# Optimization experiments

Measured on AMD Instinct MI355X. Metric: run time of the kernel, lower is better.

## Reference

```python
import jax, jax.numpy as jnp
import numpy as np

EPS = 1e-6
NUM_HEADS = 16


def setup_inputs() -> dict:
    key = jax.random.key(0)
    ks = jax.random.split(key, 11)
    B, S, E = 2, 2048, 1024
    sc = 1.0 / np.sqrt(E)
    return {
        "x": jax.random.normal(ks[0], (B, S, E), dtype=jnp.float32),
        "Wq": jax.random.normal(ks[1], (E, E), dtype=jnp.float32) * sc,
        "bq": jax.random.normal(ks[2], (E,), dtype=jnp.float32) * 0.01,
        "Wk": jax.random.normal(ks[3], (E, E), dtype=jnp.float32) * sc,
        "bk": jax.random.normal(ks[4], (E,), dtype=jnp.float32) * 0.01,
        "Wv": jax.random.normal(ks[5], (E, E), dtype=jnp.float32) * sc,
        "bv": jax.random.normal(ks[6], (E,), dtype=jnp.float32) * 0.01,
        "Wp": jax.random.normal(ks[7], (E, E), dtype=jnp.float32) * sc,
        "bp": jax.random.normal(ks[8], (E,), dtype=jnp.float32) * 0.01,
        "gain": jax.random.uniform(ks[9], (E,), dtype=jnp.float32),
        "beta": jax.random.normal(ks[10], (E,), dtype=jnp.float32),
    }


def _layer_norm(x, gain, beta):
    # torch: (x - mean) / (std + eps) * gain + bias, std with Bessel correction
    mean = jnp.mean(x, axis=-1, keepdims=True)
    std = jnp.std(x, axis=-1, keepdims=True, ddof=1)
    return (x - mean) / (std + EPS) * gain + beta


def reference(x, Wq, bq, Wk, bk, Wv, bv, Wp, bp, gain, beta):
    B, S, E = x.shape
    H = NUM_HEADS
    D = E // H
    # QKV projections, split heads: [B,S,E] -> [B,H,S,D]
    def heads(y):
        return y.reshape(B, S, H, D).transpose(0, 2, 1, 3)
    q = heads(x @ Wq + bq)
    k = heads(x @ Wk + bk)
    v = heads(x @ Wv + bv)
    # scores [B,H,S,S], mask=None path (no causal mask applied in forward)
    scores = jnp.einsum("bhid,bhjd->bhij", q, k) / jnp.sqrt(jnp.float32(D))
    attn = jax.nn.softmax(scores, axis=-1)  # dropout is identity at eval
    y = jnp.einsum("bhij,bhjd->bhid", attn, v)
    y = y.transpose(0, 2, 1, 3).reshape(B, S, E)
    return _layer_norm(y @ Wp + bp, gain, beta)
```

## Files before the change

### kernel.cpp

```cpp
#include <hip/hip_runtime.h>
#include <hip/hip_bf16.h>
#include <math.h>

constexpr int Bc = 2;
constexpr int Sc = 2048;
constexpr int Ec = 1024;
constexpr int Hc = 16;
constexpr int Dc = 64;

typedef __attribute__((ext_vector_type(8))) short short8;
typedef __attribute__((ext_vector_type(4))) short short4v;
typedef __attribute__((ext_vector_type(2))) int int2v;
typedef __attribute__((ext_vector_type(4))) float f32x4;

__device__ inline unsigned short f2bf(float x) {
    __hip_bfloat16 h = __float2bfloat16(x);
    return *reinterpret_cast<unsigned short*>(&h);
}

__device__ inline float bf2f(unsigned short u) {
    unsigned int v = (unsigned int)u << 16;
    return __builtin_bit_cast(float, v);
}

__device__ inline f32x4 mfma16(short8 a, short8 b, f32x4 c) {
    return __builtin_amdgcn_mfma_f32_16x16x32_bf16(a, b, c, 0, 0, 0);
}

__device__ inline f32x4 mfma16k16(short4v a, short4v b, f32x4 c) {
#if __has_builtin(__builtin_amdgcn_mfma_f32_16x16x16bf16_1k)
    return __builtin_amdgcn_mfma_f32_16x16x16bf16_1k(a, b, c, 0, 0, 0);
#else
    f32x4 d;
    asm("v_mfma_f32_16x16x16_bf16 %0, %1, %2, %3"
        : "=v"(d) : "v"(a), "v"(b), "v"(c));
    return d;
#endif
}

__device__ inline float exp2_fast(float x) {
    float r;
    asm("v_exp_f32 %0, %1" : "=v"(r) : "v"(x));
    return r;
}

__device__ inline int cvt_pk_bf16(float lo, float hi) {
    int r;
    asm("v_cvt_pk_bf16_f32 %0, %1, %2" : "=v"(r) : "v"(lo), "v"(hi));
    return r;
}

__device__ inline void gload_lds16(const unsigned short* gsrc, unsigned short* ldst) {
    __builtin_amdgcn_global_load_lds(
        (const __attribute__((address_space(1))) unsigned int*)(const void*)gsrc,
        (__attribute__((address_space(3))) unsigned int*)(void*)ldst,
        16, 0, 0);
}

__global__ __launch_bounds__(256) void convert_x_kernel(
    const float* __restrict__ X, unsigned short* __restrict__ Xb, int total8)
{
    int i = blockIdx.x * 256 + threadIdx.x;
    if (i >= total8) return;
    const float4* src = (const float4*)(X + (size_t)i * 8);
    float4 a = src[0], b = src[1];
    short8 o;
    o[0] = f2bf(a.x); o[1] = f2bf(a.y); o[2] = f2bf(a.z); o[3] = f2bf(a.w);
    o[4] = f2bf(b.x); o[5] = f2bf(b.y); o[6] = f2bf(b.z); o[7] = f2bf(b.w);
    *(short8*)(Xb + (size_t)i * 8) = o;
}

__global__ __launch_bounds__(256) void transpose_w_kernel(
    const float* __restrict__ W0, const float* __restrict__ W1,
    const float* __restrict__ W2, const float* __restrict__ W3,
    unsigned short* __restrict__ T0, unsigned short* __restrict__ T1,
    unsigned short* __restrict__ T2, unsigned short* __restrict__ T3)
{
    __shared__ unsigned short Ls[64][72];
    const float* W; unsigned short* T;
    switch (blockIdx.z) {
        case 0: W = W0; T = T0; break;
        case 1: W = W1; T = T1; break;
        case 2: W = W2; T = T2; break;
        default: W = W3; T = T3; break;
    }
    const int n0 = blockIdx.x * 64, k0 = blockIdx.y * 64;
    const int t = threadIdx.x;
    {
        int k = t >> 2, nb = (t & 3) * 16;
        const float* src = W + (size_t)(k0 + k) * Ec + n0 + nb;
#pragma unroll
        for (int j = 0; j < 16; ++j) Ls[k][nb + j] = f2bf(src[j]);
    }
    __syncthreads();
    {
        int n = t >> 2, kb = (t & 3) * 16;
        short8 o0, o1;
#pragma unroll
        for (int j = 0; j < 8; ++j) { o0[j] = Ls[kb + j][n]; o1[j] = Ls[kb + 8 + j][n]; }
        unsigned short* dst = T + (size_t)(n0 + n) * Ec + k0 + kb;
        *(short8*)dst = o0;
        *(short8*)(dst + 8) = o1;
    }
}

constexpr int BM = 128, BK = 64;

template<int BNt>
__device__ __forceinline__ void gemm_core_t(
    const unsigned short* __restrict__ A, const unsigned short* __restrict__ Bt,
    const float* __restrict__ bias, float* __restrict__ Cf,
    unsigned short* __restrict__ Cb, int M, int N, int K, int mode, float oscale)
{
    constexpr int NW = BNt / 32;
    constexpr int WN = BNt / 2;
    constexpr int CH = (BM + BNt) / 8;
    constexpr int PW = CH / 4;
    __shared__ unsigned short lds[2][(BM + BNt) * BK];
    const int tid = threadIdx.x, lane = tid & 63, wid = tid >> 6;
    const int c16 = lane & 15, g = lane >> 4;
    const int wr = wid >> 1, wc = wid & 1;
    const int row0 = blockIdx.y * BM, col0 = blockIdx.x * BNt;

    const int rsub = lane >> 3;
    const int colE = ((lane & 7) ^ rsub) * 8;

    f32x4 acc[4][NW] = {};

    auto stage = [&](int buf, int k0) {
        unsigned short* Ab = &lds[buf][0];
        unsigned short* Bb = &lds[buf][BM * BK];
#pragma unroll
        for (int i = 0; i < PW; ++i) {
            int c = wid * PW + i;
            if (c < 16) {
                const unsigned short* src = A + (size_t)(row0 + c * 8 + rsub) * K + k0 + colE;
                gload_lds16(src, Ab + c * 512);
            } else {
                int c2 = c - 16;
                const unsigned short* src = Bt + (size_t)(col0 + c2 * 8 + rsub) * K + k0 + colE;
                gload_lds16(src, Bb + c2 * 512);
            }
        }
    };

    stage(0, 0);
    __syncthreads();
    int cur = 0;
    const int NT = K / BK;
    for (int t = 0; t < NT; ++t) {
        if (t + 1 < NT) stage(cur ^ 1, (t + 1) * BK);
        const unsigned short* Ab = &lds[cur][0];
        const unsigned short* Bb = &lds[cur][BM * BK];
#pragma unroll
        for (int kk = 0; kk < 2; ++kk) {
            const int cb = ((kk * 64 + g * 16) ^ ((c16 & 7) << 4)) >> 1;
            short8 af[4], bfr[NW];
#pragma unroll
            for (int m = 0; m < 4; ++m) {
                int row = wr * 64 + m * 16 + c16;
                af[m] = *(const short8*)(Ab + row * BK + cb);
            }
#pragma unroll
            for (int n = 0; n < NW; ++n) {
                int row = wc * WN + n * 16 + c16;
                bfr[n] = *(const short8*)(Bb + row * BK + cb);
            }
#pragma unroll
            for (int m = 0; m < 4; ++m)
#pragma unroll
                for (int n = 0; n < NW; ++n)
                    acc[m][n] = mfma16(af[m], bfr[n], acc[m][n]);
        }
        __syncthreads();
        cur ^= 1;
    }

#pragma unroll
    for (int m = 0; m < 4; ++m) {
#pragma unroll
        for (int n = 0; n < NW; ++n) {
            int gc = col0 + wc * WN + n * 16 + c16;
            float bi = bias[gc];
            if (mode == 2) {
                int h = gc >> 6, d = gc & (Dc - 1);
                int s0 = row0 + wr * 64 + m * 16 + g * 4;
                int b = s0 >> 11, s = s0 & (Sc - 1);
                short4v pk;
#pragma unroll
                for (int r = 0; r < 4; ++r)
                    pk[r] = (short)f2bf((acc[m][n][r] + bi) * oscale);
                *(short4v*)&Cb[(((size_t)b * Hc + h) * Dc + d) * Sc + s] = pk;
            } else {
#pragma unroll
                for (int r = 0; r < 4; ++r) {
                    int gr = row0 + wr * 64 + m * 16 + g * 4 + r;
                    float v = (acc[m][n][r] + bi) * oscale;
                    if (mode == 0) {
                        Cf[(size_t)gr * N + gc] = v;
                    } else {
                        int b = gr >> 11, s = gr & (Sc - 1);
                        int h = gc >> 6, d = gc & (Dc - 1);
                        Cb[(((size_t)b * Hc + h) * Sc + s) * Dc + d] = f2bf(v);
                    }
                }
            }
        }
    }
}

__global__ __launch_bounds__(256) void gemm_mfma_kernel(
    const unsigned short* __restrict__ A, const unsigned short* __restrict__ Bt,
    const float* __restrict__ bias, float* __restrict__ Cf, int M, int N, int K)
{
    gemm_core_t<64>(A, Bt, bias, Cf, nullptr, M, N, K, 0, 1.0f);
}

__global__ __launch_bounds__(256) void qkv_gemm_kernel(
    const unsigned short* __restrict__ A,
    const unsigned short* __restrict__ WqT, const unsigned short* __restrict__ WkT,
    const unsigned short* __restrict__ WvT,
    const float* __restrict__ bq, const float* __restrict__ bk,
    const float* __restrict__ bv,
    unsigned short* __restrict__ Qb, unsigned short* __restrict__ Kb,
    unsigned short* __restrict__ Vt, int M, int N, int K, float sl2e)
{
    if (blockIdx.z == 0)      gemm_core_t<128>(A, WqT, bq, nullptr, Qb, M, N, K, 1, sl2e);
    else if (blockIdx.z == 1) gemm_core_t<128>(A, WkT, bk, nullptr, Kb, M, N, K, 1, 1.0f);
    else                      gemm_core_t<128>(A, WvT, bv, nullptr, Vt, M, N, K, 2, 1.0f);
}

__global__ __launch_bounds__(256) void attn_mfma_kernel(
    const unsigned short* __restrict__ Q, const unsigned short* __restrict__ K,
    const unsigned short* __restrict__ Vt,
    unsigned short* __restrict__ Op0, unsigned short* __restrict__ Op1,
    float* __restrict__ ls)
{
    __shared__ __align__(16) unsigned short lds[2][2][64 * 64];

    const int tid  = threadIdx.x;
    const int lane = tid & 63, wid = tid >> 6;
    const int g = lane >> 4, c16 = lane & 15;
    const int bh = blockIdx.x;
    const int qw = blockIdx.y * 128 + wid * 32;
    const int ks = blockIdx.z;
    const int kbase = ks * (Sc / 2);
    const size_t base = (size_t)bh * Sc * Dc;

    short8 bq[2][2];
#pragma unroll
    for (int u = 0; u < 2; ++u) {
        const unsigned short* Qp = Q + base + (size_t)(qw + u * 16 + c16) * Dc;
        bq[u][0] = *(const short8*)(Qp + g * 8);
        bq[u][1] = *(const short8*)(Qp + 32 + g * 8);
    }

    const int rsub = lane >> 3;
    const int srcoffE = 8 * ((lane & 7) ^ rsub);
    const int row0g = (wid * 2 + 0) * 8 + rsub;
    const int row1g = (wid * 2 + 1) * 8 + rsub;

    const unsigned short* kg0 = K  + base + (size_t)(kbase + row0g) * Dc + srcoffE;
    const unsigned short* kg1 = K  + base + (size_t)(kbase + row1g) * Dc + srcoffE;
    const unsigned short* vg0 = Vt + base + (size_t)row0g * Sc + kbase + srcoffE;
    const unsigned short* vg1 = Vt + base + (size_t)row1g * Sc + kbase + srcoffE;

    f32x4 o[2][4] = {};
    float psacc[2] = {0.f, 0.f};

    auto stage = [&](unsigned short* kbuf, unsigned short* vbuf) {
        gload_lds16(kg0, kbuf + (wid * 2 + 0) * 512);
        gload_lds16(kg1, kbuf + (wid * 2 + 1) * 512);
        gload_lds16(vg0, vbuf + (wid * 2 + 0) * 512);
        gload_lds16(vg1, vbuf + (wid * 2 + 1) * 512);
        kg0 += 64 * Dc; kg1 += 64 * Dc;
        vg0 += 64;      vg1 += 64;
    };

    const int sw = (c16 & 7) << 4;

    auto compute = [&](const unsigned short* kbuf, const unsigned short* vbuf) {
        const char* kbc = (const char*)kbuf;
        const char* vbc = (const char*)vbuf;

        f32x4 c[2][4];
        __builtin_amdgcn_s_setprio(1);
#pragma unroll
        for (int ct = 0; ct < 4; ++ct) {
            const int kr = ct * 16 + c16;
            short8 alo = *(const short8*)(kbc + kr * 128 + ((16 * g) ^ sw));
            short8 ahi = *(const short8*)(kbc + kr * 128 + ((64 + 16 * g) ^ sw));
            f32x4 z0 = {}, z1 = {};
            z0 = mfma16(alo, bq[0][0], z0);
            c[0][ct] = mfma16(ahi, bq[0][1], z0);
            z1 = mfma16(alo, bq[1][0], z1);
            c[1][ct] = mfma16(ahi, bq[1][1], z1);
        }
        __builtin_amdgcn_s_setprio(0);

        short4v pbv[2][4];
#pragma unroll
        for (int u = 0; u < 2; ++u) {
            float ps = 0.f;
#pragma unroll
            for (int ct = 0; ct < 4; ++ct) {
                float p0 = exp2_fast(c[u][ct][0]);
                float p1 = exp2_fast(c[u][ct][1]);
                float p2 = exp2_fast(c[u][ct][2]);
                float p3 = exp2_fast(c[u][ct][3]);
                ps += (p0 + p1) + (p2 + p3);
                int2v w;
                w[0] = cvt_pk_bf16(p0, p1);
                w[1] = cvt_pk_bf16(p2, p3);
                pbv[u][ct] = __builtin_bit_cast(short4v, w);
            }
            psacc[u] += ps;
        }

        __builtin_amdgcn_s_setprio(1);
#pragma unroll
        for (int dt = 0; dt < 4; ++dt) {
            const int drow = dt * 16 + c16;
#pragma unroll
            for (int ct = 0; ct < 4; ++ct) {
                short4v va = *(const short4v*)(vbc + drow * 128 + ((ct * 32 + 8 * g) ^ sw));
                o[0][dt] = mfma16k16(va, pbv[0][ct], o[0][dt]);
                o[1][dt] = mfma16k16(va, pbv[1][ct], o[1][dt]);
            }
        }
        __builtin_amdgcn_s_setprio(0);
    };

    unsigned short* k0b = &lds[0][0][0]; unsigned short* v0b = &lds[0][1][0];
    unsigned short* k1b = &lds[1][0][0]; unsigned short* v1b = &lds[1][1][0];

    constexpr int NT = (Sc / 2) / 64;
    stage(k0b, v0b);
    for (int kt = 0; kt < NT; kt += 2) {
        asm volatile("s_waitcnt vmcnt(0)" ::: "memory");
        __builtin_amdgcn_s_barrier();
        __builtin_amdgcn_sched_barrier(0);
        if (kt + 1 < NT) stage(k1b, v1b);
        compute(k0b, v0b);
        asm volatile("s_waitcnt vmcnt(0)" ::: "memory");
        __builtin_amdgcn_s_barrier();
        __builtin_amdgcn_sched_barrier(0);
        if (kt + 2 < NT) stage(k0b, v0b);
        compute(k1b, v1b);
    }

    const int b = bh >> 4, h = bh & (Hc - 1);
    unsigned short* Op = ks ? Op1 : Op0;
#pragma unroll
    for (int u = 0; u < 2; ++u) {
        float ps = psacc[u];
        ps += __shfl_xor(ps, 16);
        ps += __shfl_xor(ps, 32);
        const int qg = qw + u * 16 + c16;
        unsigned short* yrow = Op + ((size_t)b * Sc + qg) * Ec + h * Dc;
#pragma unroll
        for (int dt = 0; dt < 4; ++dt)
#pragma unroll
            for (int r = 0; r < 4; ++r)
                yrow[dt * 16 + g * 4 + r] = f2bf(o[u][dt][r]);
        if (g == 0)
            ls[((size_t)ks * (Bc * Hc) + bh) * Sc + qg] = ps;
    }
}

__global__ __launch_bounds__(256) void combine_kernel(
    const unsigned short* __restrict__ Op0, unsigned short* __restrict__ Op1,
    const float* __restrict__ ls)
{
    const int i = blockIdx.x * 256 + threadIdx.x;
    const int e4 = i * 4;
    const int bq = e4 >> 10;
    const int e  = e4 & 1023;
    const int h  = e >> 6;
    const int b  = bq >> 11, q = bq & (Sc - 1);
    const int bh = b * Hc + h;

    float l0 = ls[(size_t)bh * Sc + q];
    float l1 = ls[((size_t)(Bc * Hc) + bh) * Sc + q];
    float inv = 1.0f / (l0 + l1);

    short4v a = *(const short4v*)(Op0 + e4);
    short4v c = *(const short4v*)(Op1 + e4);
    short4v o;
#pragma unroll
    for (int j = 0; j < 4; ++j)
        o[j] = (short)f2bf((bf2f((unsigned short)a[j]) +
                            bf2f((unsigned short)c[j])) * inv);
    *(short4v*)(Op1 + e4) = o;
}

__global__ __launch_bounds__(256) void ln_kernel(
    const float* __restrict__ Z, const float* __restrict__ gain,
    const float* __restrict__ beta, float* __restrict__ out)
{
    __shared__ float red0[4];
    __shared__ float red1[4];
    const int row = blockIdx.x;
    const int t = threadIdx.x;
    const float4* z4 = (const float4*)(Z + (size_t)row * Ec);
    float4 v = z4[t];

    float s = v.x + v.y + v.z + v.w;
#pragma unroll
    for (int off = 32; off > 0; off >>= 1) s += __shfl_down(s, off);
    if ((t & 63) == 0) red0[t >> 6] = s;
    __syncthreads();
    float mean = (red0[0] + red0[1] + red0[2] + red0[3]) * (1.0f / Ec);

    float dx = v.x - mean; float vs = dx * dx;
    dx = v.y - mean; vs += dx * dx;
    dx = v.z - mean; vs += dx * dx;
    dx = v.w - mean; vs += dx * dx;
#pragma unroll
    for (int off = 32; off > 0; off >>= 1) vs += __shfl_down(vs, off);
    if ((t & 63) == 0) red1[t >> 6] = vs;
    __syncthreads();
    float var = (red1[0] + red1[1] + red1[2] + red1[3]) * (1.0f / (Ec - 1));
    float inv = 1.0f / (sqrtf(var) + 1e-6f);

    float4 g = ((const float4*)gain)[t];
    float4 bb = ((const float4*)beta)[t];
    float4 o;
    o.x = (v.x - mean) * inv * g.x + bb.x;
    o.y = (v.y - mean) * inv * g.y + bb.y;
    o.z = (v.z - mean) * inv * g.z + bb.z;
    o.w = (v.w - mean) * inv * g.w + bb.w;
    ((float4*)(out + (size_t)row * Ec))[t] = o;
}

extern "C" void kernel_launch(void* const* d_in, const int* in_sizes, int n_in,
                              void* d_out, int out_size, void* d_ws, size_t ws_size,
                              hipStream_t stream)
{
    const float* x    = (const float*)d_in[0];
    const float* Wq   = (const float*)d_in[1];
    const float* bq   = (const float*)d_in[2];
    const float* Wk   = (const float*)d_in[3];
    const float* bk   = (const float*)d_in[4];
    const float* Wv   = (const float*)d_in[5];
    const float* bv   = (const float*)d_in[6];
    const float* Wp   = (const float*)d_in[7];
    const float* bp   = (const float*)d_in[8];
    const float* gain = (const float*)d_in[9];
    const float* beta = (const float*)d_in[10];

    const int M = Bc * Sc;
    const size_t MK  = (size_t)M * Ec;
    const size_t EE  = (size_t)Ec * Ec;

    unsigned short* xb  = (unsigned short*)d_ws;
    unsigned short* wqt = xb + MK;
    unsigned short* wkt = wqt + EE;
    unsigned short* wvt = wkt + EE;
    unsigned short* wpt = wvt + EE;
    unsigned short* qb  = wpt + EE;
    unsigned short* kb  = qb + MK;
    unsigned short* vt  = kb + MK;
    unsigned short* yb  = vt + MK;
    float* ls = (float*)(yb + MK);

    float* z = (float*)qb;

    const float sl2e = 0.125f * 1.44269504f;

    convert_x_kernel<<<(int)(MK / 8 / 256), 256, 0, stream>>>(x, xb, (int)(MK / 8));
    transpose_w_kernel<<<dim3(Ec / 64, Ec / 64, 4), 256, 0, stream>>>(
        Wq, Wk, Wv, Wp, wqt, wkt, wvt, wpt);

    dim3 qkv_grid(Ec / 128, M / BM, 3);
    qkv_gemm_kernel<<<qkv_grid, 256, 0, stream>>>(
        xb, wqt, wkt, wvt, bq, bk, bv, qb, kb, vt, M, Ec, Ec, sl2e);

    dim3 attn_grid(Bc * Hc, Sc / 128, 2);
    attn_mfma_kernel<<<attn_grid, 256, 0, stream>>>(qb, kb, vt, xb, yb, ls);

    combine_kernel<<<(int)(MK / 4 / 256), 256, 0, stream>>>(xb, yb, ls);

    dim3 proj_grid(Ec / 64, M / BM);
    gemm_mfma_kernel<<<proj_grid, 256, 0, stream>>>(yb, wpt, bp, z, M, Ec, Ec);

    ln_kernel<<<M, 256, 0, stream>>>(z, gain, beta, (float*)d_out);
}
```

Before: 137.1 us.

## Double query rows per attention wave and interleave QK/exp per key tile

Each wave now handles 64 query rows instead of 32, halving the attention grid in the query dimension so every staged K/V tile in LDS is reused across twice as many queries. The QK^T MFMAs and the exp2/bf16 packing are now interleaved per key column tile rather than computed in two separate phases. This cuts K/V global and LDS traffic per query but doubles the accumulator and Q register footprint, which may lower occupancy. The grid shrinks to 512 blocks, which could leave compute units underused.

```diff
diff --git a/kernel.cpp b/kernel.cpp
--- a/kernel.cpp
+++ b/kernel.cpp
@@ -242,14 +242,14 @@
     const int lane = tid & 63, wid = tid >> 6;
     const int g = lane >> 4, c16 = lane & 15;
     const int bh = blockIdx.x;
-    const int qw = blockIdx.y * 128 + wid * 32;
+    const int qw = blockIdx.y * 256 + wid * 64;
     const int ks = blockIdx.z;
     const int kbase = ks * (Sc / 2);
     const size_t base = (size_t)bh * Sc * Dc;
 
-    short8 bq[2][2];
-#pragma unroll
-    for (int u = 0; u < 2; ++u) {
+    short8 bq[4][2];
+#pragma unroll
+    for (int u = 0; u < 4; ++u) {
         const unsigned short* Qp = Q + base + (size_t)(qw + u * 16 + c16) * Dc;
         bq[u][0] = *(const short8*)(Qp + g * 8);
         bq[u][1] = *(const short8*)(Qp + 32 + g * 8);
@@ -265,8 +265,8 @@
     const unsigned short* vg0 = Vt + base + (size_t)row0g * Sc + kbase + srcoffE;
     const unsigned short* vg1 = Vt + base + (size_t)row1g * Sc + kbase + srcoffE;
 
-    f32x4 o[2][4] = {};
-    float psacc[2] = {0.f, 0.f};
+    f32x4 o[4][4] = {};
+    float psacc[4] = {0.f, 0.f, 0.f, 0.f};
 
     auto stage = [&](unsigned short* kbuf, unsigned short* vbuf) {
         gload_lds16(kg0, kbuf + (wid * 2 + 0) * 512);
@@ -283,38 +283,33 @@
         const char* kbc = (const char*)kbuf;
         const char* vbc = (const char*)vbuf;
 
-        f32x4 c[2][4];
-        __builtin_amdgcn_s_setprio(1);
+        short4v pbv[4][4];
 #pragma unroll
         for (int ct = 0; ct < 4; ++ct) {
             const int kr = ct * 16 + c16;
             short8 alo = *(const short8*)(kbc + kr * 128 + ((16 * g) ^ sw));
             short8 ahi = *(const short8*)(kbc + kr * 128 + ((64 + 16 * g) ^ sw));
-            f32x4 z0 = {}, z1 = {};
-            z0 = mfma16(alo, bq[0][0], z0);
-            c[0][ct] = mfma16(ahi, bq[0][1], z0);
-            z1 = mfma16(alo, bq[1][0], z1);
-            c[1][ct] = mfma16(ahi, bq[1][1], z1);
-        }
-        __builtin_amdgcn_s_setprio(0);
-
-        short4v pbv[2][4];
-#pragma unroll
-        for (int u = 0; u < 2; ++u) {
-            float ps = 0.f;
-#pragma unroll
-            for (int ct = 0; ct < 4; ++ct) {
-                float p0 = exp2_fast(c[u][ct][0]);
-                float p1 = exp2_fast(c[u][ct][1]);
-                float p2 = exp2_fast(c[u][ct][2]);
-                float p3 = exp2_fast(c[u][ct][3]);
-                ps += (p0 + p1) + (p2 + p3);
+            f32x4 c4[4];
+            __builtin_amdgcn_s_setprio(1);
+#pragma unroll
+            for (int u = 0; u < 4; ++u) {
+                f32x4 z = {};
+                z = mfma16(alo, bq[u][0], z);
+                c4[u] = mfma16(ahi, bq[u][1], z);
+            }
+            __builtin_amdgcn_s_setprio(0);
+#pragma unroll
+            for (int u = 0; u < 4; ++u) {
+                float p0 = exp2_fast(c4[u][0]);
+                float p1 = exp2_fast(c4[u][1]);
+                float p2 = exp2_fast(c4[u][2]);
+                float p3 = exp2_fast(c4[u][3]);
+                psacc[u] += (p0 + p1) + (p2 + p3);
                 int2v w;
                 w[0] = cvt_pk_bf16(p0, p1);
                 w[1] = cvt_pk_bf16(p2, p3);
                 pbv[u][ct] = __builtin_bit_cast(short4v, w);
             }
-            psacc[u] += ps;
         }
 
         __builtin_amdgcn_s_setprio(1);
@@ -324,8 +319,9 @@
 #pragma unroll
             for (int ct = 0; ct < 4; ++ct) {
                 short4v va = *(const short4v*)(vbc + drow * 128 + ((ct * 32 + 8 * g) ^ sw));
-                o[0][dt] = mfma16k16(va, pbv[0][ct], o[0][dt]);
-                o[1][dt] = mfma16k16(va, pbv[1][ct], o[1][dt]);
+#pragma unroll
+                for (int u = 0; u < 4; ++u)
+                    o[u][dt] = mfma16k16(va, pbv[u][ct], o[u][dt]);
             }
         }
         __builtin_amdgcn_s_setprio(0);
@@ -352,7 +348,7 @@
     const int b = bh >> 4, h = bh & (Hc - 1);
     unsigned short* Op = ks ? Op1 : Op0;
 #pragma unroll
-    for (int u = 0; u < 2; ++u) {
+    for (int u = 0; u < 4; ++u) {
         float ps = psacc[u];
         ps += __shfl_xor(ps, 16);
         ps += __shfl_xor(ps, 32);
@@ -476,7 +472,7 @@
     qkv_gemm_kernel<<<qkv_grid, 256, 0, stream>>>(
         xb, wqt, wkt, wvt, bq, bk, bv, qb, kb, vt, M, Ec, Ec, sl2e);
 
-    dim3 attn_grid(Bc * Hc, Sc / 128, 2);
+    dim3 attn_grid(Bc * Hc, Sc / 256, 2);
     attn_mfma_kernel<<<attn_grid, 256, 0, stream>>>(qb, kb, vt, xb, yb, ls);
 
     combine_kernel<<<(int)(MK / 4 / 256), 256, 0, stream>>>(xb, yb, ls);
```

Result: slower. 141.8 us (+3.4%).

## Drop split-K attention and combine pass; merge prep kernels into one launch

Applied to the files above, without the earlier changes.

The attention kernel no longer splits the key dimension across two blocks. Each block now walks all 2048 keys and normalizes its output by the row sum before writing, so the partial-output buffers and the separate combine kernel go away. The x conversion and weight transposes are also fused into a single prep launch. This cuts a kernel launch plus the extra global traffic for partial outputs and sums, but the attention grid shrinks from 1024 to 512 blocks, which lowers parallelism on a large-CU GPU.

```diff
diff --git a/kernel.cpp b/kernel.cpp
--- a/kernel.cpp
+++ b/kernel.cpp
@@ -16,11 +16,6 @@
 __device__ inline unsigned short f2bf(float x) {
     __hip_bfloat16 h = __float2bfloat16(x);
     return *reinterpret_cast<unsigned short*>(&h);
-}
-
-__device__ inline float bf2f(unsigned short u) {
-    unsigned int v = (unsigned int)u << 16;
-    return __builtin_bit_cast(float, v);
 }
 
 __device__ inline f32x4 mfma16(short8 a, short8 b, f32x4 c) {
@@ -57,35 +52,35 @@
         16, 0, 0);
 }
 
-__global__ __launch_bounds__(256) void convert_x_kernel(
-    const float* __restrict__ X, unsigned short* __restrict__ Xb, int total8)
-{
-    int i = blockIdx.x * 256 + threadIdx.x;
-    if (i >= total8) return;
-    const float4* src = (const float4*)(X + (size_t)i * 8);
-    float4 a = src[0], b = src[1];
-    short8 o;
-    o[0] = f2bf(a.x); o[1] = f2bf(a.y); o[2] = f2bf(a.z); o[3] = f2bf(a.w);
-    o[4] = f2bf(b.x); o[5] = f2bf(b.y); o[6] = f2bf(b.z); o[7] = f2bf(b.w);
-    *(short8*)(Xb + (size_t)i * 8) = o;
-}
-
-__global__ __launch_bounds__(256) void transpose_w_kernel(
+__global__ __launch_bounds__(256) void prep_kernel(
+    const float* __restrict__ X, unsigned short* __restrict__ Xb,
     const float* __restrict__ W0, const float* __restrict__ W1,
     const float* __restrict__ W2, const float* __restrict__ W3,
     unsigned short* __restrict__ T0, unsigned short* __restrict__ T1,
     unsigned short* __restrict__ T2, unsigned short* __restrict__ T3)
 {
     __shared__ unsigned short Ls[64][72];
+    const int bid = blockIdx.x, t = threadIdx.x;
+    if (bid < 2048) {
+        int i = bid * 256 + t;
+        const float4* src = (const float4*)(X + (size_t)i * 8);
+        float4 a = src[0], b = src[1];
+        short8 o;
+        o[0] = f2bf(a.x); o[1] = f2bf(a.y); o[2] = f2bf(a.z); o[3] = f2bf(a.w);
+        o[4] = f2bf(b.x); o[5] = f2bf(b.y); o[6] = f2bf(b.z); o[7] = f2bf(b.w);
+        *(short8*)(Xb + (size_t)i * 8) = o;
+        return;
+    }
+    const int tt = bid - 2048;
     const float* W; unsigned short* T;
-    switch (blockIdx.z) {
+    switch (tt >> 8) {
         case 0: W = W0; T = T0; break;
         case 1: W = W1; T = T1; break;
         case 2: W = W2; T = T2; break;
         default: W = W3; T = T3; break;
     }
-    const int n0 = blockIdx.x * 64, k0 = blockIdx.y * 64;
-    const int t = threadIdx.x;
+    const int rem = tt & 255;
+    const int n0 = (rem & 15) * 64, k0 = (rem >> 4) * 64;
     {
         int k = t >> 2, nb = (t & 3) * 16;
         const float* src = W + (size_t)(k0 + k) * Ec + n0 + nb;
@@ -232,9 +227,7 @@
 
 __global__ __launch_bounds__(256) void attn_mfma_kernel(
     const unsigned short* __restrict__ Q, const unsigned short* __restrict__ K,
-    const unsigned short* __restrict__ Vt,
-    unsigned short* __restrict__ Op0, unsigned short* __restrict__ Op1,
-    float* __restrict__ ls)
+    const unsigned short* __restrict__ Vt, unsigned short* __restrict__ Y)
 {
     __shared__ __align__(16) unsigned short lds[2][2][64 * 64];
 
@@ -243,8 +236,6 @@
     const int g = lane >> 4, c16 = lane & 15;
     const int bh = blockIdx.x;
     const int qw = blockIdx.y * 128 + wid * 32;
-    const int ks = blockIdx.z;
-    const int kbase = ks * (Sc / 2);
     const size_t base = (size_t)bh * Sc * Dc;
 
     short8 bq[2][2];
@@ -260,10 +251,10 @@
     const int row0g = (wid * 2 + 0) * 8 + rsub;
     const int row1g = (wid * 2 + 1) * 8 + rsub;
 
-    const unsigned short* kg0 = K  + base + (size_t)(kbase + row0g) * Dc + srcoffE;
-    const unsigned short* kg1 = K  + base + (size_t)(kbase + row1g) * Dc + srcoffE;
-    const unsigned short* vg0 = Vt + base + (size_t)row0g * Sc + kbase + srcoffE;
-    const unsigned short* vg1 = Vt + base + (size_t)row1g * Sc + kbase + srcoffE;
+    const unsigned short* kg0 = K  + base + (size_t)row0g * Dc + srcoffE;
+    const unsigned short* kg1 = K  + base + (size_t)row1g * Dc + srcoffE;
+    const unsigned short* vg0 = Vt + base + (size_t)row0g * Sc + srcoffE;
+    const unsigned short* vg1 = Vt + base + (size_t)row1g * Sc + srcoffE;
 
     f32x4 o[2][4] = {};
     float psacc[2] = {0.f, 0.f};
@@ -334,7 +325,7 @@
     unsigned short* k0b = &lds[0][0][0]; unsigned short* v0b = &lds[0][1][0];
     unsigned short* k1b = &lds[1][0][0]; unsigned short* v1b = &lds[1][1][0];
 
-    constexpr int NT = (Sc / 2) / 64;
+    constexpr int NT = Sc / 64;
     stage(k0b, v0b);
     for (int kt = 0; kt < NT; kt += 2) {
         asm volatile("s_waitcnt vmcnt(0)" ::: "memory");
@@ -350,48 +341,20 @@
     }
 
     const int b = bh >> 4, h = bh & (Hc - 1);
-    unsigned short* Op = ks ? Op1 : Op0;
 #pragma unroll
     for (int u = 0; u < 2; ++u) {
         float ps = psacc[u];
         ps += __shfl_xor(ps, 16);
         ps += __shfl_xor(ps, 32);
+        const float inv = 1.f / ps;
         const int qg = qw + u * 16 + c16;
-        unsigned short* yrow = Op + ((size_t)b * Sc + qg) * Ec + h * Dc;
+        unsigned short* yrow = Y + ((size_t)b * Sc + qg) * Ec + h * Dc;
 #pragma unroll
         for (int dt = 0; dt < 4; ++dt)
 #pragma unroll
             for (int r = 0; r < 4; ++r)
-                yrow[dt * 16 + g * 4 + r] = f2bf(o[u][dt][r]);
-        if (g == 0)
-            ls[((size_t)ks * (Bc * Hc) + bh) * Sc + qg] = ps;
-    }
-}
-
-__global__ __launch_bounds__(256) void combine_kernel(
-    const unsigned short* __restrict__ Op0, unsigned short* __restrict__ Op1,
-    const float* __restrict__ ls)
-{
-    const int i = blockIdx.x * 256 + threadIdx.x;
-    const int e4 = i * 4;
-    const int bq = e4 >> 10;
-    const int e  = e4 & 1023;
-    const int h  = e >> 6;
-    const int b  = bq >> 11, q = bq & (Sc - 1);
-    const int bh = b * Hc + h;
-
-    float l0 = ls[(size_t)bh * Sc + q];
-    float l1 = ls[((size_t)(Bc * Hc) + bh) * Sc + q];
-    float inv = 1.0f / (l0 + l1);
-
-    short4v a = *(const short4v*)(Op0 + e4);
-    short4v c = *(const short4v*)(Op1 + e4);
-    short4v o;
-#pragma unroll
-    for (int j = 0; j < 4; ++j)
-        o[j] = (short)f2bf((bf2f((unsigned short)a[j]) +
-                            bf2f((unsigned short)c[j])) * inv);
-    *(short4v*)(Op1 + e4) = o;
+                yrow[dt * 16 + g * 4 + r] = f2bf(o[u][dt][r] * inv);
+    }
 }
 
 __global__ __launch_bounds__(256) void ln_kernel(
@@ -462,24 +425,19 @@
     unsigned short* kb  = qb + MK;
     unsigned short* vt  = kb + MK;
     unsigned short* yb  = vt + MK;
-    float* ls = (float*)(yb + MK);
 
     float* z = (float*)qb;
 
     const float sl2e = 0.125f * 1.44269504f;
 
-    convert_x_kernel<<<(int)(MK / 8 / 256), 256, 0, stream>>>(x, xb, (int)(MK / 8));
-    transpose_w_kernel<<<dim3(Ec / 64, Ec / 64, 4), 256, 0, stream>>>(
-        Wq, Wk, Wv, Wp, wqt, wkt, wvt, wpt);
+    prep_kernel<<<3072, 256, 0, stream>>>(x, xb, Wq, Wk, Wv, Wp, wqt, wkt, wvt, wpt);
 
     dim3 qkv_grid(Ec / 128, M / BM, 3);
     qkv_gemm_kernel<<<qkv_grid, 256, 0, stream>>>(
         xb, wqt, wkt, wvt, bq, bk, bv, qb, kb, vt, M, Ec, Ec, sl2e);
 
-    dim3 attn_grid(Bc * Hc, Sc / 128, 2);
-    attn_mfma_kernel<<<attn_grid, 256, 0, stream>>>(qb, kb, vt, xb, yb, ls);
-
-    combine_kernel<<<(int)(MK / 4 / 256), 256, 0, stream>>>(xb, yb, ls);
+    dim3 attn_grid(Bc * Hc, Sc / 128);
+    attn_mfma_kernel<<<attn_grid, 256, 0, stream>>>(qb, kb, vt, yb);
 
     dim3 proj_grid(Ec / 64, M / BM);
     gemm_mfma_kernel<<<proj_grid, 256, 0, stream>>>(yb, wpt, bp, z, M, Ec, Ec);
```

Result: faster. 127.4 us (-7.1%).
